# Optimization experiments

Measured on AMD Instinct MI355X. Metric: run time of the kernel, lower is better.

The kernel has to match this reference:

```python
import jax, jax.numpy as jnp
import numpy as np

D, F, E, K = 1024, 2752, 8, 2  # hidden, intermediate, num_experts, top-k


def setup_inputs() -> dict:
    key = jax.random.key(0)
    k0, k1, k2, k3, k4 = jax.random.split(key, 5)
    s = 0.02  # init scale to keep activations in a sane range
    x = jax.random.normal(k0, (2, 512, D), jnp.float32)
    Ws = jax.random.normal(k1, (D, E), jnp.float32) * s
    bs = jnp.zeros((E,), jnp.float32)
    Wg = jax.random.normal(k2, (E, D, F), jnp.float32) * s
    Wu = jax.random.normal(k3, (E, D, F), jnp.float32) * s
    Wd = jax.random.normal(k4, (E, F, D), jnp.float32) * s
    return {"x": x, "Ws": Ws, "bs": bs, "Wg": Wg, "Wu": Wu, "Wd": Wd}


def reference(x, Ws, bs, Wg, Wu, Wd):
    b, n, d = x.shape
    xt = x.reshape(-1, d)                      # [T, D], T = b*n
    # gating: top-k over expert logits, softmax over the selected k
    logits = xt @ Ws + bs                      # [T, E]
    topk_w, topk_idx = jax.lax.top_k(logits, K)
    topk_w = jax.nn.softmax(topk_w, axis=-1)   # [T, K]
    # combine weights: zero for unselected experts
    combine = jnp.sum(jax.nn.one_hot(topk_idx, E, dtype=xt.dtype) * topk_w[..., None], axis=1)  # [T, E]
    # per-expert SwiGLU MLP (Llama): down(silu(gate(x)) * up(x))
    g = jnp.einsum('td,edf->tef', xt, Wg)
    u = jnp.einsum('td,edf->tef', xt, Wu)
    h = jax.nn.silu(g) * u                     # [T, E, F]
    y = jnp.einsum('tef,efd->ted', h, Wd)      # [T, E, D]
    out = jnp.einsum('ted,te->td', y, combine) # weighted combine over selected experts
    return out.reshape(b, n, d)
```

## Files before the change

kernel.cpp:

```cpp
#include <hip/hip_runtime.h>

#define DH 1024
#define FH 2752
#define NE 8
#define NT 1024
#define BM 256

typedef unsigned short u16;
typedef __bf16 bf16x8 __attribute__((ext_vector_type(8)));
typedef u16 u16x8 __attribute__((ext_vector_type(8)));
typedef float f32x4 __attribute__((ext_vector_type(4)));

__device__ __forceinline__ u16 f2bf(float f) {
  unsigned int u = __float_as_uint(f);
  unsigned int r = (u + 0x7fffu + ((u >> 16) & 1u)) >> 16;
  return (u16)r;
}
__device__ __forceinline__ bf16x8 as_bf(int4 v) {
  union { int4 i; bf16x8 b; } u; u.i = v; return u.b;
}
__device__ __forceinline__ bf16x8 as_bfu(u16x8 v) {
  union { u16x8 u; bf16x8 b; } x; x.u = v; return x.b;
}

#define BAR()                                                   \
  do {                                                          \
    asm volatile("s_waitcnt lgkmcnt(0)" ::: "memory");          \
    __builtin_amdgcn_s_barrier();                               \
    asm volatile("" ::: "memory");                              \
  } while (0)

__global__ void gate_kernel(const float* __restrict__ x,
                            const float* __restrict__ Ws,
                            const float* __restrict__ bs,
                            u16* __restrict__ xb,
                            int* __restrict__ tki,
                            float* __restrict__ tkw) {
  int gtid = blockIdx.x * blockDim.x + threadIdx.x;
  int t = gtid >> 6;
  int lane = gtid & 63;
  if (t >= NT) return;
  const float* xr = x + (size_t)t * DH;
  float acc[NE];
#pragma unroll
  for (int e = 0; e < NE; ++e) acc[e] = 0.f;
  for (int d = lane; d < DH; d += 64) {
    float xv = xr[d];
    xb[(size_t)t * DH + d] = f2bf(xv);
    const float4* wr = (const float4*)(Ws + (size_t)d * NE);
    float4 w0 = wr[0], w1 = wr[1];
    acc[0] += xv * w0.x; acc[1] += xv * w0.y;
    acc[2] += xv * w0.z; acc[3] += xv * w0.w;
    acc[4] += xv * w1.x; acc[5] += xv * w1.y;
    acc[6] += xv * w1.z; acc[7] += xv * w1.w;
  }
#pragma unroll
  for (int e = 0; e < NE; ++e) {
#pragma unroll
    for (int off = 32; off > 0; off >>= 1)
      acc[e] += __shfl_xor(acc[e], off);
  }
  if (lane == 0) {
    float l[NE];
#pragma unroll
    for (int e = 0; e < NE; ++e) l[e] = acc[e] + bs[e];
    int i0 = 0;
#pragma unroll
    for (int e = 1; e < NE; ++e) if (l[e] > l[i0]) i0 = e;
    int i1 = (i0 == 0) ? 1 : 0;
#pragma unroll
    for (int e = 0; e < NE; ++e) if (e != i0 && l[e] > l[i1]) i1 = e;
    float e1 = __expf(l[i1] - l[i0]);
    float denom = 1.f + e1;
    tki[t*2]   = i0; tki[t*2+1] = i1;
    tkw[t*2]   = 1.f / denom;
    tkw[t*2+1] = e1 / denom;
  }
}

__global__ void group_kernel(const int* __restrict__ tki,
                             int* __restrict__ offs,
                             int* __restrict__ rtok,
                             int* __restrict__ posf) {
  __shared__ int cnt[NE];
  __shared__ int run[NE];
  int tid = threadIdx.x;
  if (tid < NE) cnt[tid] = 0;
  __syncthreads();
  for (int t = tid; t < NT; t += blockDim.x) {
    atomicAdd(&cnt[tki[t*2]], 1);
    atomicAdd(&cnt[tki[t*2+1]], 1);
  }
  __syncthreads();
  if (tid == 0) {
    int r = 0;
    for (int e = 0; e < NE; ++e) { offs[e] = r; run[e] = r; r += cnt[e]; }
    offs[NE] = r;
  }
  __syncthreads();
  for (int t = tid; t < NT; t += blockDim.x) {
    for (int k = 0; k < 2; ++k) {
      int e = tki[t*2+k];
      int p = atomicAdd(&run[e], 1);
      rtok[p] = t;
      posf[t*2+k] = p;
    }
  }
}

#define GU_LOADA(AS, KT)                                                     \
  { _Pragma("unroll") for (int mf = 0; mf < 4; ++mf) {                       \
      AS[mf][0] = *(const int4*)(aptr[mf] + (KT)*64);                        \
      AS[mf][1] = *(const int4*)(aptr[mf] + (KT)*64 + 32);                   \
  } }

#define GU_LOADB(BS, KT)                                                     \
  { const float* gp_ = gsrc + (size_t)(KT)*64*FH;                            \
    const float* up_ = usrc + (size_t)(KT)*64*FH;                            \
    _Pragma("unroll") for (int r_ = 0; r_ < 4; ++r_) {                       \
      BS##g[r_] = *(const float2*)(gp_ + (size_t)r_*FH);                     \
      BS##u[r_] = *(const float2*)(up_ + (size_t)r_*FH);                     \
  } }

#define GU_WRITEB(BS, BUF)                                                   \
  { _Pragma("unroll") for (int j_ = 0; j_ < 2; ++j_) {                       \
      union { u16 s[4]; uint2 v; } pg_, pu_;                                 \
      _Pragma("unroll") for (int r_ = 0; r_ < 4; ++r_) {                     \
        pg_.s[r_] = f2bf(j_ ? BS##g[r_].y : BS##g[r_].x);                    \
        pu_.s[r_] = f2bf(j_ ? BS##u[r_].y : BS##u[r_].x);                    \
      }                                                                      \
      *(uint2*)&bg_sm[BUF][2*cc + j_][4*gg] = pg_.v;                         \
      *(uint2*)&bu_sm[BUF][2*cc + j_][4*gg] = pu_.v;                         \
  } }

#define GU_READF(CUR)                                                        \
  { _Pragma("unroll") for (int h_ = 0; h_ < 2; ++h_) {                       \
      fg[h_][0] = *(const u16x8*)&bg_sm[CUR][nl][h_*32 + kg];                \
      fg[h_][1] = *(const u16x8*)&bg_sm[CUR][16 + nl][h_*32 + kg];           \
      fu[h_][0] = *(const u16x8*)&bu_sm[CUR][nl][h_*32 + kg];                \
      fu[h_][1] = *(const u16x8*)&bu_sm[CUR][16 + nl][h_*32 + kg];           \
  } }

#define GU_MFMA(AS)                                                          \
  { _Pragma("unroll") for (int h_ = 0; h_ < 2; ++h_) {                       \
      _Pragma("unroll") for (int mf = 0; mf < 4; ++mf) {                     \
        bf16x8 av = as_bf(AS[mf][h_]);                                       \
        accg[mf][0] = __builtin_amdgcn_mfma_f32_16x16x32_bf16(av, as_bfu(fg[h_][0]), accg[mf][0], 0,0,0); \
        accg[mf][1] = __builtin_amdgcn_mfma_f32_16x16x32_bf16(av, as_bfu(fg[h_][1]), accg[mf][1], 0,0,0); \
        accu[mf][0] = __builtin_amdgcn_mfma_f32_16x16x32_bf16(av, as_bfu(fu[h_][0]), accu[mf][0], 0,0,0); \
        accu[mf][1] = __builtin_amdgcn_mfma_f32_16x16x32_bf16(av, as_bfu(fu[h_][1]), accu[mf][1], 0,0,0); \
  } } }

#define GU_BODY(ACUR, ANXT, BSW, BSI, CUR, IT, DO_NEXT, DO_ISSUE, DO_BAR)    \
  { if (DO_NEXT)  GU_LOADA(ANXT, (IT)+1);                                    \
    if (DO_ISSUE) GU_LOADB(BSI, (IT)+2);                                     \
    u16x8 fg[2][2], fu[2][2];                                                \
    GU_READF(CUR);                                                           \
    if (DO_NEXT) { GU_WRITEB(BSW, (CUR)^1); }                                \
    GU_MFMA(ACUR);                                                           \
    if (DO_BAR) BAR();                                                       \
  }

__global__ __launch_bounds__(256, 2)
void gu_kernel(const u16* __restrict__ xb,
               const float* __restrict__ Wg,
               const float* __restrict__ Wu,
               u16* __restrict__ hbuf,
               const int* __restrict__ offs,
               const int* __restrict__ rtok) {
  __shared__ u16 bg_sm[2][32][68];
  __shared__ u16 bu_sm[2][32][68];

  int e  = blockIdx.z;
  int mt = blockIdx.y;
  int nt = blockIdx.x;
  int off0 = offs[e];
  int cnt  = offs[e+1] - off0;
  if (cnt <= 0 || mt * BM >= cnt) return;
  int p0 = off0 + mt * BM;
  int rmax = cnt - mt * BM - 1;
  int n0 = nt * 32;
  int tid = threadIdx.x;
  int lane = tid & 63, wv = tid >> 6;
  int kg = (lane >> 4) * 8;
  int nl = lane & 15;

  const u16* aptr[4];
#pragma unroll
  for (int mf = 0; mf < 4; ++mf) {
    int lrow = wv*64 + nl + mf*16;
    int tok = rtok[p0 + (lrow > rmax ? rmax : lrow)];
    aptr[mf] = xb + (size_t)tok * DH + kg;
  }

  int cc = tid & 15;
  int gg = tid >> 4;
  const float* gsrc = Wg + (size_t)e * DH * FH + (size_t)(4*gg) * FH + n0 + 2*cc;
  const float* usrc = Wu + (size_t)e * DH * FH + (size_t)(4*gg) * FH + n0 + 2*cc;

  f32x4 accg[4][2], accu[4][2];
#pragma unroll
  for (int mf = 0; mf < 4; ++mf)
#pragma unroll
    for (int nf = 0; nf < 2; ++nf) {
      accg[mf][nf] = f32x4{0.f,0.f,0.f,0.f};
      accu[mf][nf] = f32x4{0.f,0.f,0.f,0.f};
    }

  int4 A0[4][2], A1[4][2];
  float2 BAg[4], BAu[4], BBg[4], BBu[4];

  GU_LOADB(BA, 0);
  GU_LOADA(A0, 0);
  GU_WRITEB(BA, 0);
  GU_LOADB(BB, 1);
  BAR();

  for (int t = 0; t < 16; t += 2) {
    GU_BODY(A0, A1, BB, BA, 0, t,     1,            (t+2 < 16),   1);
    GU_BODY(A1, A0, BA, BB, 1, (t+1), (t+2 < 16),   (t+3 < 16),   (t+2 < 16));
  }

#pragma unroll
  for (int mf = 0; mf < 4; ++mf) {
    int lr0 = wv*64 + (lane >> 4)*4 + mf*16;
#pragma unroll
    for (int nf = 0; nf < 2; ++nf) {
      int col = n0 + nf*16 + nl;
#pragma unroll
      for (int q = 0; q < 4; ++q) {
        int lrow = lr0 + q;
        if (lrow <= rmax) {
          float g = accg[mf][nf][q], u = accu[mf][nf][q];
          float s = g / (1.f + __expf(-g));
          hbuf[(size_t)(p0 + lrow) * FH + col] = f2bf(s * u);
        }
      }
    }
  }
}

#define DN_LOADA(AS, KT)                                                     \
  { _Pragma("unroll") for (int mf = 0; mf < 4; ++mf) {                       \
      AS[mf][0] = *(const int4*)(aptr[mf] + (KT)*64);                        \
      AS[mf][1] = *(const int4*)(aptr[mf] + (KT)*64 + 32);                   \
  } }

#define DN_LOADB(BS, KT)                                                     \
  { const float* dp_ = dsrc + (size_t)(KT)*64*DH;                            \
    _Pragma("unroll") for (int r_ = 0; r_ < 4; ++r_)                         \
      BS##d[r_] = *(const float2*)(dp_ + (size_t)r_*DH);                     \
  }

#define DN_WRITEB(BS, BUF)                                                   \
  { _Pragma("unroll") for (int j_ = 0; j_ < 2; ++j_) {                       \
      union { u16 s[4]; uint2 v; } pd_;                                      \
      _Pragma("unroll") for (int r_ = 0; r_ < 4; ++r_)                       \
        pd_.s[r_] = f2bf(j_ ? BS##d[r_].y : BS##d[r_].x);                    \
      *(uint2*)&bd_sm[BUF][2*cc + j_][4*gg] = pd_.v;                         \
  } }

#define DN_BODY(ACUR, ANXT, BSW, BSI, CUR, IT, DO_NEXT, DO_ISSUE, DO_BAR)    \
  { if (DO_NEXT)  DN_LOADA(ANXT, (IT)+1);                                    \
    if (DO_ISSUE) DN_LOADB(BSI, (IT)+2);                                     \
    u16x8 fd[2][2];                                                          \
    _Pragma("unroll") for (int h_ = 0; h_ < 2; ++h_) {                       \
      fd[h_][0] = *(const u16x8*)&bd_sm[CUR][nl][h_*32 + kg];                \
      fd[h_][1] = *(const u16x8*)&bd_sm[CUR][16 + nl][h_*32 + kg];           \
    }                                                                        \
    if (DO_NEXT) { DN_WRITEB(BSW, (CUR)^1); }                                \
    _Pragma("unroll") for (int h_ = 0; h_ < 2; ++h_) {                       \
      _Pragma("unroll") for (int mf = 0; mf < 4; ++mf) {                     \
        bf16x8 av = as_bf(ACUR[mf][h_]);                                     \
        acc[mf][0] = __builtin_amdgcn_mfma_f32_16x16x32_bf16(av, as_bfu(fd[h_][0]), acc[mf][0], 0,0,0); \
        acc[mf][1] = __builtin_amdgcn_mfma_f32_16x16x32_bf16(av, as_bfu(fd[h_][1]), acc[mf][1], 0,0,0); \
      } }                                                                    \
    if (DO_BAR) BAR();                                                       \
  }

__global__ __launch_bounds__(256, 2)
void dn_kernel(const u16* __restrict__ hb,
               const float* __restrict__ Wd,
               float* __restrict__ y,
               const int* __restrict__ offs) {
  __shared__ u16 bd_sm[2][32][68];

  int e  = blockIdx.z;
  int mt = blockIdx.y;
  int bx = blockIdx.x;
  int nt = bx & 31;
  int ks = bx >> 5;
  int kt0   = ks ? 1408 : 0;
  int nIter = ks ? 21 : 22;
  int off0 = offs[e];
  int cnt  = offs[e+1] - off0;
  if (cnt <= 0 || mt * BM >= cnt) return;
  int p0 = off0 + mt * BM;
  int rmax = cnt - mt * BM - 1;
  int n0 = nt * 32;
  int tid = threadIdx.x;
  int lane = tid & 63, wv = tid >> 6;
  int kg = (lane >> 4) * 8;
  int nl = lane & 15;

  const u16* aptr[4];
#pragma unroll
  for (int mf = 0; mf < 4; ++mf) {
    int lrow = wv*64 + nl + mf*16;
    int arow = p0 + (lrow > rmax ? rmax : lrow);
    aptr[mf] = hb + (size_t)arow * FH + kt0 + kg;
  }

  int cc = tid & 15;
  int gg = tid >> 4;
  const float* dsrc = Wd + (size_t)e * FH * DH + (size_t)(kt0 + 4*gg) * DH + n0 + 2*cc;

  f32x4 acc[4][2];
#pragma unroll
  for (int mf = 0; mf < 4; ++mf)
#pragma unroll
    for (int nf = 0; nf < 2; ++nf)
      acc[mf][nf] = f32x4{0.f,0.f,0.f,0.f};

  int4 A0[4][2], A1[4][2];
  float2 BAd[4], BBd[4];

  DN_LOADB(BA, 0);
  DN_LOADA(A0, 0);
  DN_WRITEB(BA, 0);
  DN_LOADB(BB, 1);
  BAR();

  int it = 0;
  for (; it + 2 <= nIter; it += 2) {
    DN_BODY(A0, A1, BB, BA, 0, it,     (it+1 < nIter), (it+2 < nIter), 1);
    DN_BODY(A1, A0, BA, BB, 1, (it+1), (it+2 < nIter), (it+3 < nIter), (it+2 < nIter));
  }
  if (it < nIter) {
    DN_BODY(A0, A1, BB, BA, 0, it, 0, 0, 0);
  }

  float* yout = y + (size_t)ks * 2048 * DH;
#pragma unroll
  for (int mf = 0; mf < 4; ++mf) {
    int lr0 = wv*64 + (lane >> 4)*4 + mf*16;
#pragma unroll
    for (int nf = 0; nf < 2; ++nf) {
      int col = n0 + nf*16 + nl;
#pragma unroll
      for (int q = 0; q < 4; ++q) {
        int lrow = lr0 + q;
        if (lrow <= rmax)
          yout[(size_t)(p0 + lrow) * DH + col] = acc[mf][nf][q];
      }
    }
  }
}

__global__ void combine_kernel(const float* __restrict__ y,
                               const float* __restrict__ tkw,
                               const int* __restrict__ posf,
                               float* __restrict__ out) {
  int t = blockIdx.x;
  int d = threadIdx.x;
  const float* y1 = y + (size_t)2048 * DH;
  int pa = posf[t*2], pb = posf[t*2+1];
  float wa = tkw[t*2], wb = tkw[t*2+1];
  f32x4 a0 = ((const f32x4*)(y  + (size_t)pa * DH))[d];
  f32x4 a1 = ((const f32x4*)(y1 + (size_t)pa * DH))[d];
  f32x4 b0 = ((const f32x4*)(y  + (size_t)pb * DH))[d];
  f32x4 b1 = ((const f32x4*)(y1 + (size_t)pb * DH))[d];
  f32x4 o;
#pragma unroll
  for (int i = 0; i < 4; ++i)
    o[i] = wa*(a0[i]+a1[i]) + wb*(b0[i]+b1[i]);
  ((f32x4*)(out + (size_t)t * DH))[d] = o;
}

extern "C" void kernel_launch(void* const* d_in, const int* in_sizes, int n_in,
                              void* d_out, int out_size, void* d_ws, size_t ws_size,
                              hipStream_t stream) {
  const float* x  = (const float*)d_in[0];
  const float* Ws = (const float*)d_in[1];
  const float* bs = (const float*)d_in[2];
  const float* Wg = (const float*)d_in[3];
  const float* Wu = (const float*)d_in[4];
  const float* Wd = (const float*)d_in[5];
  float* out = (float*)d_out;
  char* ws = (char*)d_ws;

  int*   tki  = (int*)  (ws + 0);
  float* tkw  = (float*)(ws + 8192);
  int*   offs = (int*)  (ws + 16384);
  int*   posf = (int*)  (ws + 20480);
  int*   rtok = (int*)  (ws + 28672);
  u16*   xb   = (u16*)  (ws + 36864);
  char*  base2 = ws + 36864 + 2097152;
  u16*   hbuf = (u16*)(base2);
  float* yws  = (float*)(base2 + 11272192);

  gate_kernel<<<256, 256, 0, stream>>>(x, Ws, bs, xb, tki, tkw);
  group_kernel<<<1, 256, 0, stream>>>(tki, offs, rtok, posf);
  gu_kernel<<<dim3(FH/32, 4, NE), 256, 0, stream>>>(xb, Wg, Wu, hbuf, offs, rtok);
  dn_kernel<<<dim3(64, 4, NE), 256, 0, stream>>>(hbuf, Wd, yws, offs);
  combine_kernel<<<NT, 256, 0, stream>>>(yws, tkw, posf, out);
}
```

Measured before the change: 191.0 us.

## Compact expert-tile grid via tile table and XCD-aware block remapping

The group kernel now writes a compact table of (expert, m-tile) pairs, padded to 16 entries. The gate-up and down kernels switch to a 1D grid that indexes this table, so the grid no longer carries a fixed 4 m-tiles per expert, most of which returned early. Block ids are permuted with a stride of 8 so that blocks sharing an expert or tile land on the same XCD, which is meant to improve L2 reuse of weights. Launch bounds rise to 4 waves per SIMD, which may force register spills.

```diff
diff --git a/kernel.cpp b/kernel.cpp
--- a/kernel.cpp
+++ b/kernel.cpp
@@ -81,7 +81,8 @@
 __global__ void group_kernel(const int* __restrict__ tki,
                              int* __restrict__ offs,
                              int* __restrict__ rtok,
-                             int* __restrict__ posf) {
+                             int* __restrict__ posf,
+                             unsigned* __restrict__ ttab) {
   __shared__ int cnt[NE];
   __shared__ int run[NE];
   int tid = threadIdx.x;
@@ -96,6 +97,12 @@
     int r = 0;
     for (int e = 0; e < NE; ++e) { offs[e] = r; run[e] = r; r += cnt[e]; }
     offs[NE] = r;
+    int idx = 0;
+    for (int e = 0; e < NE; ++e) {
+      int nt256 = (cnt[e] + 255) >> 8;
+      for (int m = 0; m < nt256; ++m) ttab[idx++] = ((unsigned)e << 16) | (unsigned)m;
+    }
+    for (; idx < 16; ++idx) ttab[idx] = 0xFFFFFFFFu;
   }
   __syncthreads();
   for (int t = tid; t < NT; t += blockDim.x) {
@@ -161,25 +168,29 @@
     if (DO_BAR) BAR();                                                       \
   }
 
-__global__ __launch_bounds__(256, 2)
+__global__ __launch_bounds__(256, 4)
 void gu_kernel(const u16* __restrict__ xb,
                const float* __restrict__ Wg,
                const float* __restrict__ Wu,
                u16* __restrict__ hbuf,
                const int* __restrict__ offs,
-               const int* __restrict__ rtok) {
+               const int* __restrict__ rtok,
+               const unsigned* __restrict__ ttab) {
   __shared__ u16 bg_sm[2][32][68];
   __shared__ u16 bu_sm[2][32][68];
 
-  int e  = blockIdx.z;
-  int mt = blockIdx.y;
-  int nt = blockIdx.x;
+  int bid = blockIdx.x;
+  int work = (bid & 7) * 172 + (bid >> 3);
+  int mt = work & 15;
+  int ntile = work >> 4;
+  unsigned tv = ttab[mt];
+  if (tv == 0xFFFFFFFFu) return;
+  int e = tv >> 16, mtl = tv & 0xFFFF;
   int off0 = offs[e];
   int cnt  = offs[e+1] - off0;
-  if (cnt <= 0 || mt * BM >= cnt) return;
-  int p0 = off0 + mt * BM;
-  int rmax = cnt - mt * BM - 1;
-  int n0 = nt * 32;
+  int p0 = off0 + mtl * BM;
+  int rmax = cnt - mtl * BM - 1;
+  int n0 = ntile * 32;
   int tid = threadIdx.x;
   int lane = tid & 63, wv = tid >> 6;
   int kg = (lane >> 4) * 8;
@@ -207,18 +218,18 @@
       accu[mf][nf] = f32x4{0.f,0.f,0.f,0.f};
     }
 
-  int4 A0[4][2], A1[4][2];
+  int4 a0[4][2], a1[4][2];
   float2 BAg[4], BAu[4], BBg[4], BBu[4];
 
   GU_LOADB(BA, 0);
-  GU_LOADA(A0, 0);
+  GU_LOADA(a0, 0);
   GU_WRITEB(BA, 0);
   GU_LOADB(BB, 1);
   BAR();
 
   for (int t = 0; t < 16; t += 2) {
-    GU_BODY(A0, A1, BB, BA, 0, t,     1,            (t+2 < 16),   1);
-    GU_BODY(A1, A0, BA, BB, 1, (t+1), (t+2 < 16),   (t+3 < 16),   (t+2 < 16));
+    GU_BODY(a0, a1, BB, BA, 0, t,     1,            (t+2 < 16),   1);
+    GU_BODY(a1, a0, BA, BB, 1, (t+1), (t+2 < 16),   (t+3 < 16),   (t+2 < 16));
   }
 
 #pragma unroll
@@ -260,43 +271,47 @@
       *(uint2*)&bd_sm[BUF][2*cc + j_][4*gg] = pd_.v;                         \
   } }
 
-#define DN_BODY(ACUR, ANXT, BSW, BSI, CUR, IT, DO_NEXT, DO_ISSUE, DO_BAR)    \
-  { if (DO_NEXT)  DN_LOADA(ANXT, (IT)+1);                                    \
-    if (DO_ISSUE) DN_LOADB(BSI, (IT)+2);                                     \
+#define DN_BODY(ACUR, ANXT, BSW, BSI, CUR, IT)                               \
+  { bool dn_ = (IT) + 1 < nIter;                                             \
+    if (dn_)             DN_LOADA(ANXT, (IT)+1);                             \
+    if ((IT)+2 < nIter)  DN_LOADB(BSI, (IT)+2);                              \
     u16x8 fd[2][2];                                                          \
     _Pragma("unroll") for (int h_ = 0; h_ < 2; ++h_) {                       \
       fd[h_][0] = *(const u16x8*)&bd_sm[CUR][nl][h_*32 + kg];                \
       fd[h_][1] = *(const u16x8*)&bd_sm[CUR][16 + nl][h_*32 + kg];           \
     }                                                                        \
-    if (DO_NEXT) { DN_WRITEB(BSW, (CUR)^1); }                                \
+    if (dn_) { DN_WRITEB(BSW, (CUR)^1); }                                    \
     _Pragma("unroll") for (int h_ = 0; h_ < 2; ++h_) {                       \
       _Pragma("unroll") for (int mf = 0; mf < 4; ++mf) {                     \
         bf16x8 av = as_bf(ACUR[mf][h_]);                                     \
         acc[mf][0] = __builtin_amdgcn_mfma_f32_16x16x32_bf16(av, as_bfu(fd[h_][0]), acc[mf][0], 0,0,0); \
         acc[mf][1] = __builtin_amdgcn_mfma_f32_16x16x32_bf16(av, as_bfu(fd[h_][1]), acc[mf][1], 0,0,0); \
       } }                                                                    \
-    if (DO_BAR) BAR();                                                       \
-  }
-
-__global__ __launch_bounds__(256, 2)
+    if (dn_) BAR();                                                          \
+  }
+
+__global__ __launch_bounds__(256, 4)
 void dn_kernel(const u16* __restrict__ hb,
                const float* __restrict__ Wd,
                float* __restrict__ y,
-               const int* __restrict__ offs) {
+               const int* __restrict__ offs,
+               const unsigned* __restrict__ ttab) {
   __shared__ u16 bd_sm[2][32][68];
 
-  int e  = blockIdx.z;
-  int mt = blockIdx.y;
-  int bx = blockIdx.x;
-  int nt = bx & 31;
-  int ks = bx >> 5;
+  int bid = blockIdx.x;
+  int work = (bid & 7) * 128 + (bid >> 3);
+  int mt = work & 15;
+  int nt = (work >> 4) & 31;
+  int ks = work >> 9;
   int kt0   = ks ? 1408 : 0;
   int nIter = ks ? 21 : 22;
+  unsigned tv = ttab[mt];
+  if (tv == 0xFFFFFFFFu) return;
+  int e = tv >> 16, mtl = tv & 0xFFFF;
   int off0 = offs[e];
   int cnt  = offs[e+1] - off0;
-  if (cnt <= 0 || mt * BM >= cnt) return;
-  int p0 = off0 + mt * BM;
-  int rmax = cnt - mt * BM - 1;
+  int p0 = off0 + mtl * BM;
+  int rmax = cnt - mtl * BM - 1;
   int n0 = nt * 32;
   int tid = threadIdx.x;
   int lane = tid & 63, wv = tid >> 6;
@@ -322,22 +337,22 @@
     for (int nf = 0; nf < 2; ++nf)
       acc[mf][nf] = f32x4{0.f,0.f,0.f,0.f};
 
-  int4 A0[4][2], A1[4][2];
+  int4 a0[4][2], a1[4][2];
   float2 BAd[4], BBd[4];
 
   DN_LOADB(BA, 0);
-  DN_LOADA(A0, 0);
+  DN_LOADA(a0, 0);
   DN_WRITEB(BA, 0);
   DN_LOADB(BB, 1);
   BAR();
 
   int it = 0;
   for (; it + 2 <= nIter; it += 2) {
-    DN_BODY(A0, A1, BB, BA, 0, it,     (it+1 < nIter), (it+2 < nIter), 1);
-    DN_BODY(A1, A0, BA, BB, 1, (it+1), (it+2 < nIter), (it+3 < nIter), (it+2 < nIter));
+    DN_BODY(a0, a1, BB, BA, 0, it);
+    DN_BODY(a1, a0, BA, BB, 1, (it+1));
   }
   if (it < nIter) {
-    DN_BODY(A0, A1, BB, BA, 0, it, 0, 0, 0);
+    DN_BODY(a0, a1, BB, BA, 0, it);
   }
 
   float* yout = y + (size_t)ks * 2048 * DH;
@@ -389,19 +404,20 @@
   float* out = (float*)d_out;
   char* ws = (char*)d_ws;
 
-  int*   tki  = (int*)  (ws + 0);
-  float* tkw  = (float*)(ws + 8192);
-  int*   offs = (int*)  (ws + 16384);
-  int*   posf = (int*)  (ws + 20480);
-  int*   rtok = (int*)  (ws + 28672);
-  u16*   xb   = (u16*)  (ws + 36864);
-  char*  base2 = ws + 36864 + 2097152;
-  u16*   hbuf = (u16*)(base2);
-  float* yws  = (float*)(base2 + 11272192);
+  int*      tki  = (int*)     (ws + 0);
+  float*    tkw  = (float*)   (ws + 8192);
+  int*      offs = (int*)     (ws + 16384);
+  unsigned* ttab = (unsigned*)(ws + 16640);
+  int*      posf = (int*)     (ws + 20480);
+  int*      rtok = (int*)     (ws + 28672);
+  u16*      xb   = (u16*)     (ws + 36864);
+  char*     base2 = ws + 36864 + 2097152;
+  u16*      hbuf = (u16*)(base2);
+  float*    yws  = (float*)(base2 + 11272192);
 
   gate_kernel<<<256, 256, 0, stream>>>(x, Ws, bs, xb, tki, tkw);
-  group_kernel<<<1, 256, 0, stream>>>(tki, offs, rtok, posf);
-  gu_kernel<<<dim3(FH/32, 4, NE), 256, 0, stream>>>(xb, Wg, Wu, hbuf, offs, rtok);
-  dn_kernel<<<dim3(64, 4, NE), 256, 0, stream>>>(hbuf, Wd, yws, offs);
+  group_kernel<<<1, 256, 0, stream>>>(tki, offs, rtok, posf, ttab);
+  gu_kernel<<<1376, 256, 0, stream>>>(xb, Wg, Wu, hbuf, offs, rtok, ttab);
+  dn_kernel<<<1024, 256, 0, stream>>>(hbuf, Wd, yws, offs, ttab);
   combine_kernel<<<NT, 256, 0, stream>>>(yws, tkw, posf, out);
 }
```

Measured after the change: 746.8 us. +291.1%, slower.
